# Kernel tuning notes

Hardware: AMD Instinct MI355X
Metric: run time of the kernel (lower is better)

Reference implementation:

```python
import jax, jax.numpy as jnp
import numpy as np

EPS = 1e-12  # F.normalize default eps

def _l2norm(a, axis):
    n = jnp.sqrt(jnp.sum(a * a, axis=axis, keepdims=True))
    return a / jnp.maximum(n, EPS)

def setup_inputs() -> dict:
    key = jax.random.key(0)
    kx, kc = jax.random.split(key)
    x = jax.random.normal(kx, (32, 64, 64, 64), dtype=jnp.float32)        # [B,C,H,W]
    codebook = 0.2 * jax.random.normal(kc, (512, 64), dtype=jnp.float32)  # nn.init.normal_(w, 0, 0.2)
    return {"x": x, "codebook": codebook}

def reference(x, codebook):
    # mode == 'angular': normalize codebook rows and x along dim=1 (channels)
    cb = _l2norm(codebook, axis=1)          # [K,C]
    xn = _l2norm(x, axis=1)                 # [B,C,H,W]
    # x.transpose(-1, dim) with dim=1 -> swap axes 1 and 3
    xt = jnp.swapaxes(xn, 1, -1)            # [B,W,H,C]
    B, W, H, C = xt.shape
    flat = xt.reshape(-1, C)                # [N,C]
    d = (jnp.sum(cb * cb, axis=1)[None, :]
         + jnp.sum(flat * flat, axis=1, keepdims=True)
         - 2.0 * flat @ cb.T)               # [N,K]
    idx = jnp.argmin(d, axis=1)             # [N]
    codes = cb[idx].reshape(B, W, H, C)
    indices = idx.reshape(B, W, H)
    codes = jnp.swapaxes(codes, 1, -1)      # back to [B,C,H,W]
    indices = jnp.swapaxes(indices, 1, -1)  # [B,H,W]
    return codes, indices
```

## Files before the change

kernel.cpp:

```cpp
#include <hip/hip_runtime.h>

#define VQ_EPS    1e-12f
#define VQ_WINDOW 0.01f
#define VQ_CAP    12

typedef short bf16x8 __attribute__((ext_vector_type(8)));
typedef float f32x4  __attribute__((ext_vector_type(4)));

static __device__ __forceinline__ unsigned short f2bf(float f) {
    unsigned u = __float_as_uint(f);
    u += 0x7fffu + ((u >> 16) & 1u);
    return (unsigned short)(u >> 16);
}

static __device__ __forceinline__ unsigned f2ord(float f) {
    unsigned b = __float_as_uint(f);
    return (b & 0x80000000u) ? ~b : (b | 0x80000000u);
}

static __device__ __forceinline__ void wave_lds_fence() {
    asm volatile("s_waitcnt lgkmcnt(0)" ::: "memory");
}

static __device__ __forceinline__ unsigned umed3(unsigned a, unsigned b, unsigned c) {
    unsigned d;
    asm("v_med3_u32 %0, %1, %2, %3" : "=v"(d) : "v"(a), "v"(b), "v"(c));
    return d;
}

__global__ __launch_bounds__(64) void cb_prep_kernel(const float* __restrict__ cb,
                                                     float* __restrict__ cbn,
                                                     unsigned short* __restrict__ cbB,
                                                     float* __restrict__ kn2,
                                                     float* __restrict__ kn2p) {
    const int k = blockIdx.x;
    const int c = threadIdx.x;
    float v = cb[k * 64 + c];
    float s = v * v;
    #pragma unroll
    for (int off = 32; off > 0; off >>= 1) s += __shfl_xor(s, off, 64);
    float n = sqrtf(s);
    float cn = v / fmaxf(n, VQ_EPS);
    cbn[k * 64 + c] = cn;

    const int ntile = k >> 4, col = k & 15;
    const int ks = c >> 5, quad = (c >> 3) & 3, j = c & 7;
    cbB[(((ntile * 2 + ks) * 64) + quad * 16 + col) * 8 + j] = f2bf(cn);

    float s2 = cn * cn;
    #pragma unroll
    for (int off = 32; off > 0; off >>= 1) s2 += __shfl_xor(s2, off, 64);
    if (c == 0) { kn2[k] = s2; kn2p[k] = s2 + 2.0f; }
}

__global__ __launch_bounds__(1024, 8) void vq_mfma_kernel(const float* __restrict__ x,
                                                      const float* __restrict__ cbn,
                                                      const unsigned short* __restrict__ cbB,
                                                      const float* __restrict__ kn2,
                                                      const float* __restrict__ kn2p,
                                                      float* __restrict__ codes,
                                                      float* __restrict__ idxout) {
    __shared__ __align__(16) unsigned short lcb[32768];
    __shared__ unsigned long long spack[256];
    __shared__ int slist[256][VQ_CAP];
    __shared__ int scnt[256];

    const int t    = threadIdx.x;
    const int lane = t & 63;
    const int wid  = t >> 6;
    const int col  = lane & 15;
    const int quad = lane >> 4;
    const int wr   = wid & 3;
    const int rsel = wid >> 2;
    const int wpix = wr * 16 + col;
    const int pbase = rsel * 64;
    const int pslot = pbase + wpix;

    const int rowid = blockIdx.x * 4 + rsel;
    const int b = rowid >> 6;
    const int h = rowid & 63;
    const float* xblk = x + ((size_t)b << 18) + (h << 6);

    if (quad == 0) { scnt[pslot] = 0; spack[pslot] = 0xFFFFFFFFFFFFFFFFull; }

    float xv[16];
    #pragma unroll
    for (int ks = 0; ks < 2; ++ks)
        #pragma unroll
        for (int j = 0; j < 8; ++j)
            xv[ks * 8 + j] = xblk[(size_t)(ks * 32 + quad * 8 + j) * 4096 + wpix];

    {
        const uint4* g4 = (const uint4*)cbB;
        uint4*       l4 = (uint4*)lcb;
        #pragma unroll
        for (int r = 0; r < 4; ++r) l4[r * 1024 + t] = g4[r * 1024 + t];
    }

    float ssp = 0.0f;
    #pragma unroll
    for (int i = 0; i < 16; ++i) ssp = fmaf(xv[i], xv[i], ssp);
    ssp += __shfl_xor(ssp, 16);
    ssp += __shfl_xor(ssp, 32);
    const float m2a = -2.0f * (1.0f / fmaxf(sqrtf(ssp), VQ_EPS));
    float m2r[4];
    #pragma unroll
    for (int r = 0; r < 4; ++r) m2r[r] = __shfl(m2a, quad * 4 + r);
    const float m2P = __shfl(m2a, lane >> 2);

    bf16x8 afrag[2];
    #pragma unroll
    for (int ks = 0; ks < 2; ++ks)
        #pragma unroll
        for (int j = 0; j < 8; ++j)
            ((unsigned short*)&afrag[ks])[j] = f2bf(xv[ks * 8 + j]);

    __syncthreads();

    const bf16x8* lBf = (const bf16x8*)lcb;

    unsigned run1[4] = {0xFFFFFFFFu, 0xFFFFFFFFu, 0xFFFFFFFFu, 0xFFFFFFFFu};
    unsigned run2[4] = {0xFFFFFFFFu, 0xFFFFFFFFu, 0xFFFFFFFFu, 0xFFFFFFFFu};
    unsigned run3[4] = {0xFFFFFFFFu, 0xFFFFFFFFu, 0xFFFFFFFFu, 0xFFFFFFFFu};
    #pragma unroll 4
    for (int nt = 0; nt < 32; ++nt) {
        bf16x8 b0 = lBf[(nt * 2 + 0) * 64 + lane];
        bf16x8 b1 = lBf[(nt * 2 + 1) * 64 + lane];
        f32x4 c = {0.0f, 0.0f, 0.0f, 0.0f};
        c = __builtin_amdgcn_mfma_f32_16x16x32_bf16(afrag[0], b0, c, 0, 0, 0);
        c = __builtin_amdgcn_mfma_f32_16x16x32_bf16(afrag[1], b1, c, 0, 0, 0);
        const float    kn   = kn2p[nt * 16 + col];
        const unsigned kidx = (unsigned)(nt * 16 + col);
        #pragma unroll
        for (int r = 0; r < 4; ++r) {
            float s = fmaf(m2r[r], c[r], kn);
            unsigned key = (__float_as_uint(s) & 0xFFFFFE00u) | kidx;
            unsigned o1 = run1[r], o2 = run2[r];
            run1[r] = min(o1, key);
            run2[r] = umed3(o1, key, o2);
            run3[r] = umed3(o2, key, run3[r]);
        }
    }

    float thr[4];
    #pragma unroll
    for (int r = 0; r < 4; ++r) {
        unsigned v = run1[r];
        v = min(v, (unsigned)__shfl_xor((int)v, 1));
        v = min(v, (unsigned)__shfl_xor((int)v, 2));
        v = min(v, (unsigned)__shfl_xor((int)v, 4));
        v = min(v, (unsigned)__shfl_xor((int)v, 8));
        thr[r] = __uint_as_float(v & 0xFFFFFE00u) + VQ_WINDOW;
    }

    bool f = false;
    #pragma unroll
    for (int r = 0; r < 4; ++r)
        f |= (__uint_as_float(run3[r] & 0xFFFFFE00u) <= thr[r]);
    const unsigned long long waveflag = __ballot(f);

    if (waveflag != 0ull) {
        #pragma unroll 4
        for (int nt = 0; nt < 32; ++nt) {
            bf16x8 b0 = lBf[(nt * 2 + 0) * 64 + lane];
            bf16x8 b1 = lBf[(nt * 2 + 1) * 64 + lane];
            f32x4 c = {0.0f, 0.0f, 0.0f, 0.0f};
            c = __builtin_amdgcn_mfma_f32_16x16x32_bf16(afrag[0], b0, c, 0, 0, 0);
            c = __builtin_amdgcn_mfma_f32_16x16x32_bf16(afrag[1], b1, c, 0, 0, 0);
            const float kn   = kn2p[nt * 16 + col];
            const int   kidx = nt * 16 + col;
            #pragma unroll
            for (int r = 0; r < 4; ++r) {
                float s = fmaf(m2r[r], c[r], kn);
                if (s <= thr[r]) {
                    int pix = pbase + wr * 16 + quad * 4 + r;
                    int pos = atomicAdd(&scnt[pix], 1);
                    if (pos < VQ_CAP) slist[pix][pos] = kidx;
                }
            }
        }
    } else {
        #pragma unroll
        for (int r = 0; r < 4; ++r) {
            float s1 = __uint_as_float(run1[r] & 0xFFFFFE00u);
            if (s1 <= thr[r]) {
                int pix = pbase + wr * 16 + quad * 4 + r;
                int pos = atomicAdd(&scnt[pix], 1);
                if (pos < VQ_CAP) slist[pix][pos] = (int)(run1[r] & 0x1FFu);
            }
            float s2 = __uint_as_float(run2[r] & 0xFFFFFE00u);
            if (s2 <= thr[r]) {
                int pix = pbase + wr * 16 + quad * 4 + r;
                int pos = atomicAdd(&scnt[pix], 1);
                if (pos < VQ_CAP) slist[pix][pos] = (int)(run2[r] & 0x1FFu);
            }
        }
    }
    wave_lds_fence();

    {
        const int pw   = wr * 16 + (lane >> 2);
        const int P    = pbase + pw;
        const int sub  = lane & 3;
        const int cnt  = scnt[P];
        if (cnt > 1) {
            const float* xp = xblk + pw;
            if (cnt <= VQ_CAP) {
                for (int i = sub; i < cnt; i += 4) {
                    const int k = slist[P][i];
                    const float* cr = cbn + (size_t)k * 64;
                    float dot = 0.0f;
                    #pragma unroll 8
                    for (int c = 0; c < 64; ++c)
                        dot = fmaf(xp[(size_t)c * 4096], cr[c], dot);
                    float s = fmaf(m2P, dot, kn2[k]);
                    unsigned long long key =
                        ((unsigned long long)f2ord(s) << 32) | (unsigned)k;
                    atomicMin(&spack[P], key);
                }
            } else {
                for (int k = sub; k < 512; k += 4) {
                    const float* cr = cbn + (size_t)k * 64;
                    float dot = 0.0f;
                    #pragma unroll 8
                    for (int c = 0; c < 64; ++c)
                        dot = fmaf(xp[(size_t)c * 4096], cr[c], dot);
                    float s = fmaf(m2P, dot, kn2[k]);
                    unsigned long long key =
                        ((unsigned long long)f2ord(s) << 32) | (unsigned)k;
                    atomicMin(&spack[P], key);
                }
            }
        }
    }
    wave_lds_fence();

    const int cntw = scnt[pslot];
    const int bk = (cntw == 1) ? slist[pslot][0]
                               : (int)(spack[pslot] & 0xFFFFFFFFull);

    if (quad == 0) idxout[rowid * 64 + wpix] = (float)bk;

    {
        const float4* crow = (const float4*)(cbn + (size_t)bk * 64) + quad * 4;
        float* cp = codes + ((size_t)b << 18) + (h << 6) + wpix;
        #pragma unroll
        for (int q = 0; q < 4; ++q) {
            float4 v = crow[q];
            const int c0 = quad * 16 + q * 4;
            cp[(size_t)(c0 + 0) * 4096] = v.x;
            cp[(size_t)(c0 + 1) * 4096] = v.y;
            cp[(size_t)(c0 + 2) * 4096] = v.z;
            cp[(size_t)(c0 + 3) * 4096] = v.w;
        }
    }
}

extern "C" void kernel_launch(void* const* d_in, const int* in_sizes, int n_in,
                              void* d_out, int out_size, void* d_ws, size_t ws_size,
                              hipStream_t stream) {
    const float* x  = (const float*)d_in[0];
    const float* cb = (const float*)d_in[1];

    float*          cbn  = (float*)d_ws;
    unsigned short* cbB  = (unsigned short*)(cbn + 512 * 64);
    float*          kn2  = (float*)(cbB + 32768);
    float*          kn2p = kn2 + 512;

    float* codes  = (float*)d_out;
    float* idxout = codes + (size_t)32 * 64 * 64 * 64;

    cb_prep_kernel<<<512, 64, 0, stream>>>(cb, cbn, cbB, kn2, kn2p);
    vq_mfma_kernel<<<512, 1024, 0, stream>>>(x, cbn, cbB, kn2, kn2p, codes, idxout);
}
```

Baseline: 113.8 us.

## Split VQ kernel into MFMA scan and separate exact-refine/write kernel

Splits the fused VQ kernel in two. A scan kernel computes bf16 MFMA distances and writes per-pixel candidate lists, counts and scale factors to workspace. A finish kernel with small blocks then does exact fp32 rescoring of the candidates and writes codes and indices. The aim is to move the irregular refinement and strided output stores out of the large 1024-thread block so they get better occupancy and load balance. The cost is an extra launch, a workspace round-trip, and a second read of x. The old fused path is kept as a fallback when the workspace is too small.

```diff
diff --git a/kernel.cpp b/kernel.cpp
--- a/kernel.cpp
+++ b/kernel.cpp
@@ -51,6 +51,244 @@
     #pragma unroll
     for (int off = 32; off > 0; off >>= 1) s2 += __shfl_xor(s2, off, 64);
     if (c == 0) { kn2[k] = s2; kn2p[k] = s2 + 2.0f; }
+}
+
+__global__ __launch_bounds__(1024, 8) void vq_scan_kernel(const float* __restrict__ x,
+                                                      const unsigned short* __restrict__ cbB,
+                                                      const float* __restrict__ kn2p,
+                                                      int* __restrict__ pcnt,
+                                                      float* __restrict__ pm2,
+                                                      unsigned short* __restrict__ pcand) {
+    __shared__ __align__(16) unsigned short lcb[32768];
+    __shared__ int slist[256][VQ_CAP];
+    __shared__ int scnt[256];
+
+    const int t    = threadIdx.x;
+    const int lane = t & 63;
+    const int wid  = t >> 6;
+    const int col  = lane & 15;
+    const int quad = lane >> 4;
+    const int wr   = wid & 3;
+    const int rsel = wid >> 2;
+    const int wpix = wr * 16 + col;
+    const int pbase = rsel * 64;
+    const int pslot = pbase + wpix;
+
+    const int rowid = blockIdx.x * 4 + rsel;
+    const int b = rowid >> 6;
+    const int h = rowid & 63;
+    const float* xblk = x + ((size_t)b << 18) + (h << 6);
+
+    if (quad == 0) scnt[pslot] = 0;
+
+    float xv[16];
+    #pragma unroll
+    for (int ks = 0; ks < 2; ++ks)
+        #pragma unroll
+        for (int j = 0; j < 8; ++j)
+            xv[ks * 8 + j] = xblk[(size_t)(ks * 32 + quad * 8 + j) * 4096 + wpix];
+
+    {
+        const uint4* g4 = (const uint4*)cbB;
+        uint4*       l4 = (uint4*)lcb;
+        #pragma unroll
+        for (int r = 0; r < 4; ++r) l4[r * 1024 + t] = g4[r * 1024 + t];
+    }
+
+    float ssp = 0.0f;
+    #pragma unroll
+    for (int i = 0; i < 16; ++i) ssp = fmaf(xv[i], xv[i], ssp);
+    ssp += __shfl_xor(ssp, 16);
+    ssp += __shfl_xor(ssp, 32);
+    const float m2a = -2.0f * (1.0f / fmaxf(sqrtf(ssp), VQ_EPS));
+    float m2r[4];
+    #pragma unroll
+    for (int r = 0; r < 4; ++r) m2r[r] = __shfl(m2a, quad * 4 + r);
+
+    bf16x8 afrag[2];
+    #pragma unroll
+    for (int ks = 0; ks < 2; ++ks)
+        #pragma unroll
+        for (int j = 0; j < 8; ++j)
+            ((unsigned short*)&afrag[ks])[j] = f2bf(xv[ks * 8 + j]);
+
+    __syncthreads();
+
+    const bf16x8* lBf = (const bf16x8*)lcb;
+
+    unsigned run1[4] = {0xFFFFFFFFu, 0xFFFFFFFFu, 0xFFFFFFFFu, 0xFFFFFFFFu};
+    unsigned run2[4] = {0xFFFFFFFFu, 0xFFFFFFFFu, 0xFFFFFFFFu, 0xFFFFFFFFu};
+    unsigned run3[4] = {0xFFFFFFFFu, 0xFFFFFFFFu, 0xFFFFFFFFu, 0xFFFFFFFFu};
+    #pragma unroll 4
+    for (int nt = 0; nt < 32; ++nt) {
+        bf16x8 b0 = lBf[(nt * 2 + 0) * 64 + lane];
+        bf16x8 b1 = lBf[(nt * 2 + 1) * 64 + lane];
+        f32x4 c = {0.0f, 0.0f, 0.0f, 0.0f};
+        c = __builtin_amdgcn_mfma_f32_16x16x32_bf16(afrag[0], b0, c, 0, 0, 0);
+        c = __builtin_amdgcn_mfma_f32_16x16x32_bf16(afrag[1], b1, c, 0, 0, 0);
+        const float    kn   = kn2p[nt * 16 + col];
+        const unsigned kidx = (unsigned)(nt * 16 + col);
+        #pragma unroll
+        for (int r = 0; r < 4; ++r) {
+            float s = fmaf(m2r[r], c[r], kn);
+            unsigned key = (__float_as_uint(s) & 0xFFFFFE00u) | kidx;
+            unsigned o1 = run1[r], o2 = run2[r];
+            run1[r] = min(o1, key);
+            run2[r] = umed3(o1, key, o2);
+            run3[r] = umed3(o2, key, run3[r]);
+        }
+    }
+
+    float thr[4];
+    #pragma unroll
+    for (int r = 0; r < 4; ++r) {
+        unsigned v = run1[r];
+        v = min(v, (unsigned)__shfl_xor((int)v, 1));
+        v = min(v, (unsigned)__shfl_xor((int)v, 2));
+        v = min(v, (unsigned)__shfl_xor((int)v, 4));
+        v = min(v, (unsigned)__shfl_xor((int)v, 8));
+        thr[r] = __uint_as_float(v & 0xFFFFFE00u) + VQ_WINDOW;
+    }
+
+    bool f = false;
+    #pragma unroll
+    for (int r = 0; r < 4; ++r)
+        f |= (__uint_as_float(run3[r] & 0xFFFFFE00u) <= thr[r]);
+    const unsigned long long waveflag = __ballot(f);
+
+    if (waveflag != 0ull) {
+        #pragma unroll 4
+        for (int nt = 0; nt < 32; ++nt) {
+            bf16x8 b0 = lBf[(nt * 2 + 0) * 64 + lane];
+            bf16x8 b1 = lBf[(nt * 2 + 1) * 64 + lane];
+            f32x4 c = {0.0f, 0.0f, 0.0f, 0.0f};
+            c = __builtin_amdgcn_mfma_f32_16x16x32_bf16(afrag[0], b0, c, 0, 0, 0);
+            c = __builtin_amdgcn_mfma_f32_16x16x32_bf16(afrag[1], b1, c, 0, 0, 0);
+            const float kn   = kn2p[nt * 16 + col];
+            const int   kidx = nt * 16 + col;
+            #pragma unroll
+            for (int r = 0; r < 4; ++r) {
+                float s = fmaf(m2r[r], c[r], kn);
+                if (s <= thr[r]) {
+                    int pix = pbase + wr * 16 + quad * 4 + r;
+                    int pos = atomicAdd(&scnt[pix], 1);
+                    if (pos < VQ_CAP) slist[pix][pos] = kidx;
+                }
+            }
+        }
+    } else {
+        #pragma unroll
+        for (int r = 0; r < 4; ++r) {
+            float s1 = __uint_as_float(run1[r] & 0xFFFFFE00u);
+            if (s1 <= thr[r]) {
+                int pix = pbase + wr * 16 + quad * 4 + r;
+                int pos = atomicAdd(&scnt[pix], 1);
+                if (pos < VQ_CAP) slist[pix][pos] = (int)(run1[r] & 0x1FFu);
+            }
+            float s2 = __uint_as_float(run2[r] & 0xFFFFFE00u);
+            if (s2 <= thr[r]) {
+                int pix = pbase + wr * 16 + quad * 4 + r;
+                int pos = atomicAdd(&scnt[pix], 1);
+                if (pos < VQ_CAP) slist[pix][pos] = (int)(run2[r] & 0x1FFu);
+            }
+        }
+    }
+    wave_lds_fence();
+
+    if (quad == 0) {
+        const int gpix = rowid * 64 + wpix;
+        const int cnt  = scnt[pslot];
+        pcnt[gpix] = cnt;
+        pm2[gpix]  = m2a;
+        const int m = min(cnt, VQ_CAP);
+        unsigned short* pc = pcand + (size_t)gpix * VQ_CAP;
+        for (int i = 0; i < m; ++i) pc[i] = (unsigned short)slist[pslot][i];
+    }
+}
+
+__global__ __launch_bounds__(256) void vq_finish_kernel(const float* __restrict__ x,
+                                                      const float* __restrict__ cbn,
+                                                      const float* __restrict__ kn2,
+                                                      const int* __restrict__ pcnt,
+                                                      const float* __restrict__ pm2,
+                                                      const unsigned short* __restrict__ pcand,
+                                                      float* __restrict__ codes,
+                                                      float* __restrict__ idxout) {
+    __shared__ unsigned long long spack[64];
+
+    const int t    = threadIdx.x;
+    const int lane = t & 63;
+    const int wid  = t >> 6;
+    const int col  = lane & 15;
+    const int quad = lane >> 4;
+    const int gbase = (blockIdx.x * 4 + wid) * 16;
+    const int pslot = wid * 16 + col;
+
+    if (quad == 0) spack[pslot] = 0xFFFFFFFFFFFFFFFFull;
+
+    {
+        const int gp   = gbase + (lane >> 2);
+        const int sub  = lane & 3;
+        const int slot = wid * 16 + (lane >> 2);
+        const int cnt  = pcnt[gp];
+        if (cnt > 1) {
+            const float m2P = pm2[gp];
+            const int w = gp & 63, rowid = gp >> 6;
+            const int b = rowid >> 6, h = rowid & 63;
+            const float* xp = x + ((size_t)b << 18) + (h << 6) + w;
+            if (cnt <= VQ_CAP) {
+                const unsigned short* pc = pcand + (size_t)gp * VQ_CAP;
+                for (int i = sub; i < cnt; i += 4) {
+                    const int k = pc[i];
+                    const float* cr = cbn + (size_t)k * 64;
+                    float dot = 0.0f;
+                    #pragma unroll 8
+                    for (int c = 0; c < 64; ++c)
+                        dot = fmaf(xp[(size_t)c * 4096], cr[c], dot);
+                    float s = fmaf(m2P, dot, kn2[k]);
+                    unsigned long long key =
+                        ((unsigned long long)f2ord(s) << 32) | (unsigned)k;
+                    atomicMin(&spack[slot], key);
+                }
+            } else {
+                for (int k = sub; k < 512; k += 4) {
+                    const float* cr = cbn + (size_t)k * 64;
+                    float dot = 0.0f;
+                    #pragma unroll 8
+                    for (int c = 0; c < 64; ++c)
+                        dot = fmaf(xp[(size_t)c * 4096], cr[c], dot);
+                    float s = fmaf(m2P, dot, kn2[k]);
+                    unsigned long long key =
+                        ((unsigned long long)f2ord(s) << 32) | (unsigned)k;
+                    atomicMin(&spack[slot], key);
+                }
+            }
+        }
+    }
+    wave_lds_fence();
+
+    const int gp_e = gbase + col;
+    const int cntw = pcnt[gp_e];
+    const int bk = (cntw == 1) ? (int)pcand[(size_t)gp_e * VQ_CAP]
+                               : (int)(spack[pslot] & 0xFFFFFFFFull);
+
+    if (quad == 0) idxout[gp_e] = (float)bk;
+
+    {
+        const int w = gp_e & 63, rowid = gp_e >> 6;
+        const int b = rowid >> 6, h = rowid & 63;
+        const float4* crow = (const float4*)(cbn + (size_t)bk * 64) + quad * 4;
+        float* cp = codes + ((size_t)b << 18) + (h << 6) + w;
+        #pragma unroll
+        for (int q = 0; q < 4; ++q) {
+            float4 v = crow[q];
+            const int c0 = quad * 16 + q * 4;
+            cp[(size_t)(c0 + 0) * 4096] = v.x;
+            cp[(size_t)(c0 + 1) * 4096] = v.y;
+            cp[(size_t)(c0 + 2) * 4096] = v.z;
+            cp[(size_t)(c0 + 3) * 4096] = v.w;
+        }
+    }
 }
 
 __global__ __launch_bounds__(1024, 8) void vq_mfma_kernel(const float* __restrict__ x,
@@ -262,14 +500,26 @@
     const float* x  = (const float*)d_in[0];
     const float* cb = (const float*)d_in[1];
 
-    float*          cbn  = (float*)d_ws;
-    unsigned short* cbB  = (unsigned short*)(cbn + 512 * 64);
-    float*          kn2  = (float*)(cbB + 32768);
-    float*          kn2p = kn2 + 512;
+    char* ws = (char*)d_ws;
+    float*          cbn  = (float*)(ws + 0);
+    unsigned short* cbB  = (unsigned short*)(ws + 131072);
+    float*          kn2  = (float*)(ws + 196608);
+    float*          kn2p = (float*)(ws + 198656);
+    int*            pcnt  = (int*)(ws + 200704);
+    float*          pm2   = (float*)(ws + 724992);
+    unsigned short* pcand = (unsigned short*)(ws + 1249280);
+    const size_t WS_NEEDED = 1249280 + 3145728;
 
     float* codes  = (float*)d_out;
     float* idxout = codes + (size_t)32 * 64 * 64 * 64;
 
     cb_prep_kernel<<<512, 64, 0, stream>>>(cb, cbn, cbB, kn2, kn2p);
-    vq_mfma_kernel<<<512, 1024, 0, stream>>>(x, cbn, cbB, kn2, kn2p, codes, idxout);
-}
+    if (ws_size >= WS_NEEDED) {
+        vq_scan_kernel<<<512, 1024, 0, stream>>>(x, cbB, kn2p, pcnt, pm2, pcand);
+        vq_finish_kernel<<<2048, 256, 0, stream>>>(x, cbn, kn2, pcnt, pm2, pcand,
+                                                   codes, idxout);
+    } else {
+        vq_mfma_kernel<<<512, 1024, 0, stream>>>(x, cbn, cbB, kn2, kn2p,
+                                                 codes, idxout);
+    }
+}
```

Result: slower. 120.0 us (+5.5%).
